# Performance work log

Hardware: AMD Instinct MI355X
Metric: run time of the kernel (lower is better)

Reference implementation:

```python
import jax, jax.numpy as jnp
import numpy as np

TEMPERATURE = 0.5  # set externally on the torch module; fixed here
EPS = 1e-10

B, NPTS, NDIM = 8, 1024, 64
K, S = 16, 512  # n_clusters, book_size


def setup_inputs() -> dict:
    key = jax.random.key(0)
    k1, k2, k3, k4 = jax.random.split(key, 4)
    ze = jax.random.normal(k1, (B, NPTS, NDIM), dtype=jnp.float32)
    # per-sample cluster probabilities (rows sum to 1)
    c_probs = jax.nn.softmax(jax.random.normal(k2, (B, K), dtype=jnp.float32), axis=-1)
    books = jax.random.normal(k3, (K, S, NDIM), dtype=jnp.float32)
    log_param_q = jnp.asarray(np.log(1.0), dtype=jnp.float32)  # param_q_init = 1.0
    gumbel_u = jax.random.uniform(k4, (B, K, NPTS, S), dtype=jnp.float32)
    return {"ze": ze, "c_probs": c_probs, "books": books,
            "log_param_q": log_param_q, "gumbel_u": gumbel_u}


def reference(ze, c_probs, books, log_param_q, gumbel_u):
    # precision of the Gaussian quantizer
    precision_q = 0.5 / jnp.clip(jnp.exp(log_param_q), 1e-10)
    # squared euclidean distances: [b, k, n, s]
    d = (jnp.sum(ze * ze, axis=-1)[:, None, :, None]
         + jnp.sum(books * books, axis=-1)[None, :, None, :]
         - 2.0 * jnp.einsum('bnd,ksd->bkns', ze, books))
    logits = -d * precision_q                                   # [b,k,n,s]
    # gumbel-softmax sample (training branch)
    g = -jnp.log(-jnp.log(gumbel_u + EPS) + EPS)
    encodings = jax.nn.softmax((logits + g) / TEMPERATURE, axis=-1)
    # soft codebook lookup, mixed over clusters by per-sample c_probs
    zq = jnp.einsum('bkns,ksd,bk->bnd', encodings, books, c_probs)
    prob = jax.nn.softmax(logits, axis=-1)
    log_prob = jax.nn.log_softmax(logits, axis=-1)
    return (zq, precision_q, prob, log_prob)
```

## Files before the change

kernel.cpp:

```cpp
#include <hip/hip_runtime.h>
#include <hip/hip_bf16.h>

typedef __attribute__((ext_vector_type(8))) short short8;
typedef __attribute__((ext_vector_type(4))) float f32x4;
typedef __attribute__((ext_vector_type(2))) float f32x2;

#define WS_ZE     0u
#define WS_ZELO   (1u<<20)
#define WS_B1H    (2u<<20)
#define WS_B1L    (3u<<20)
#define WS_B2     (4u<<20)
#define WS_ZN2    (5u<<20)
#define WS_BS2    ((5u<<20)+32768u)
#define WS_ZQP    (6u<<20)

__device__ __forceinline__ unsigned short f2bf(float x) {
  __hip_bfloat16 h = __float2bfloat16(x);
  return __builtin_bit_cast(unsigned short, h);
}
__device__ __forceinline__ float bf2f(unsigned short u) {
  union { unsigned int i; float f; } x; x.i = ((unsigned int)u) << 16; return x.f;
}
__device__ __forceinline__ void lds_barrier() {
  asm volatile("s_waitcnt lgkmcnt(0)" ::: "memory");
  __builtin_amdgcn_s_barrier();
}

__global__ __launch_bounds__(256) void prep_all_k(const float* __restrict__ ze,
                                                  const float* __restrict__ books,
                                                  const float* __restrict__ lpq,
                                                  char* __restrict__ ws,
                                                  float* __restrict__ d_out) {
  const int bb = blockIdx.x;
  if (bb < 32) {
    int t = bb * 256 + threadIdx.x;
    const f32x4* row = (const f32x4*)(ze + t * 64);
    unsigned short* dh = (unsigned short*)(ws + WS_ZE) + t * 64;
    unsigned short* dl = (unsigned short*)(ws + WS_ZELO) + t * 64;
    float s = 0.f;
#pragma unroll
    for (int c = 0; c < 8; ++c) {
      const f32x4 v0 = row[2 * c], v1 = row[2 * c + 1];
      union { unsigned short u[8]; short8 v; } H, L;
#pragma unroll
      for (int r = 0; r < 4; ++r) {
        float a = v0[r]; s += a * a;
        unsigned short h = f2bf(a); H.u[r] = h; L.u[r] = f2bf(a - bf2f(h));
        float b = v1[r]; s += b * b;
        unsigned short h2 = f2bf(b); H.u[4 + r] = h2; L.u[4 + r] = f2bf(b - bf2f(h2));
      }
      *(short8*)(dh + c * 8) = H.v;
      *(short8*)(dl + c * 8) = L.v;
    }
    ((float*)(ws + WS_ZN2))[t] = s;
  } else if (bb < 64) {
    int t = (bb - 32) * 256 + threadIdx.x;
    if (t == 0) d_out[524288] = 0.5f / fmaxf(expf(lpq[0]), 1e-10f);
    const f32x4* row = (const f32x4*)(books + t * 64);
    float s = 0.f;
#pragma unroll
    for (int c = 0; c < 16; ++c) {
      const f32x4 v = row[c];
#pragma unroll
      for (int r = 0; r < 4; ++r) s += v[r] * v[r];
    }
    ((float*)(ws + WS_BS2))[t] = s;
  } else if (bb < 320) {
    int t = (bb - 64) * 256 + threadIdx.x;
    const int sl = t & 15, g = (t >> 4) & 3, f = (t >> 6) & 1, tt = (t >> 7) & 31, k = t >> 12;
    const float* src = books + ((k * 512 + tt * 16 + sl) * 64 + f * 32 + g * 8);
    const f32x4 v0 = *(const f32x4*)(src);
    const f32x4 v1 = *(const f32x4*)(src + 4);
    union { unsigned short u[8]; short8 v; } H, L;
#pragma unroll
    for (int r = 0; r < 4; ++r) {
      unsigned short h = f2bf(v0[r]); H.u[r] = h; L.u[r] = f2bf(v0[r] - bf2f(h));
      unsigned short h2 = f2bf(v1[r]); H.u[4 + r] = h2; L.u[4 + r] = f2bf(v1[r] - bf2f(h2));
    }
    const int off = (k * 32 + tt) * 2048 + f * 1024 + (sl + g * 16) * 16;
    *(short8*)(ws + WS_B1H + off) = H.v;
    *(short8*)(ws + WS_B1L + off) = L.v;
  } else {
    int t = (bb - 320) * 256 + threadIdx.x;
    const int l15 = t & 15, sub = (t >> 4) & 3, m = (t >> 6) & 3, w = (t >> 8) & 7,
              hh = (t >> 11) & 1, k = t >> 12;
    const float* src = books + ((k * 512 + hh * 256 + w * 32 + sub * 8) * 64 + m * 16 + l15);
    union { unsigned short u[8]; short8 v; } H;
#pragma unroll
    for (int j = 0; j < 8; ++j) H.u[j] = f2bf(src[j * 64]);
    *(short8*)(ws + WS_B2 + k * 65536 + ((hh * 8 + w) * 4 + m) * 1024 + (l15 + sub * 16) * 16) = H.v;
  }
}

__global__ __launch_bounds__(256) void zq_red_k(const char* __restrict__ ws,
                                                float* __restrict__ d_out) {
  int t = blockIdx.x * 256 + threadIdx.x;
  const f32x4 a = *(const f32x4*)(ws + WS_ZQP + t * 16);
  const f32x4 b = *(const f32x4*)(ws + WS_ZQP + (2u << 20) + t * 16);
  const f32x4 c = *(const f32x4*)(ws + WS_ZQP + (4u << 20) + t * 16);
  *(f32x4*)(d_out + t * 4) = a + b + c;
}

__global__ __launch_bounds__(512, 3)
void gvq_main(const float* __restrict__ gum, const float* __restrict__ cprobs,
              const float* __restrict__ lpq, char* __restrict__ ws,
              float* __restrict__ d_out) {
  __shared__ char lds[50240];
  char* lgb  = lds;
  char* encb = lds + 33024;
  float* scr_esc = (float*)(lds + 50176);

  const int tid  = threadIdx.x;
  const int lane = tid & 63;
  const int wave = tid >> 6;
  const int l15  = lane & 15;
  const int g4   = lane >> 4;

  const int bid = blockIdx.x;
  const unsigned kg = (unsigned)bid % 3u;
  const int bt  = (int)((unsigned)bid / 3u);
  const int b   = bt >> 6;
  const int n0  = (bt & 63) * 16;
  const int kbeg = (kg == 0) ? 0 : (kg == 1 ? 6 : 11);
  const int kcnt = (kg == 0) ? 6 : 5;

  const float prec  = 0.5f / fmaxf(expf(lpq[0]), 1e-10f);
  const float prec2 = 2.0f * prec;
  const float C24   = 3.7751345442790977e-11f;

  const unsigned short* zh = (const unsigned short*)(ws + WS_ZE)   + (b * 1024 + n0 + l15) * 64;
  const unsigned short* zl = (const unsigned short*)(ws + WS_ZELO) + (b * 1024 + n0 + l15) * 64;
  const short8 zf0h = *(const short8*)(zh + g4 * 8);
  const short8 zf1h = *(const short8*)(zh + 32 + g4 * 8);
  const short8 zf0l = *(const short8*)(zl + g4 * 8);
  const short8 zf1l = *(const short8*)(zl + 32 + g4 * 8);
  const float zn2p = ((const float*)(ws + WS_ZN2))[b * 1024 + n0 + l15] * prec;

  f32x4 zacc[4] = {{0,0,0,0},{0,0,0,0},{0,0,0,0},{0,0,0,0}};

  const int nr0 = wave * 2, nr1 = wave * 2 + 1;

#pragma unroll 1
  for (int kk = 0; kk < kcnt; ++kk) {
    const int k = kbeg + kk;
    const float cp = cprobs[b * 16 + k];
    const char* b1h = ws + WS_B1H + k * 65536;
    const char* b1l = ws + WS_B1L + k * 65536;
    const char* b2  = ws + WS_B2  + k * 65536;
    const float* bs2k = (const float*)(ws + WS_BS2) + k * 512;
    const long row0 = ((long)((b * 16 + k) * 1024) + n0 + nr0) * 512;
    const long row1 = ((long)((b * 16 + k) * 1024) + n0 + nr1) * 512;

#pragma unroll
    for (int i = 0; i < 4; ++i) {
      const int t = wave * 4 + i;
      const char* bh = b1h + t * 2048 + lane * 16;
      const char* bl = b1l + t * 2048 + lane * 16;
      const short8 a0h = *(const short8*)(bh);
      const short8 a1h = *(const short8*)(bh + 1024);
      const short8 a0l = *(const short8*)(bl);
      const short8 a1l = *(const short8*)(bl + 1024);
      f32x4 c = {0.f, 0.f, 0.f, 0.f};
      c = __builtin_amdgcn_mfma_f32_16x16x32_bf16(a0h, zf0h, c, 0, 0, 0);
      c = __builtin_amdgcn_mfma_f32_16x16x32_bf16(a1h, zf1h, c, 0, 0, 0);
      c = __builtin_amdgcn_mfma_f32_16x16x32_bf16(a0h, zf0l, c, 0, 0, 0);
      c = __builtin_amdgcn_mfma_f32_16x16x32_bf16(a1h, zf1l, c, 0, 0, 0);
      c = __builtin_amdgcn_mfma_f32_16x16x32_bf16(a0l, zf0h, c, 0, 0, 0);
      c = __builtin_amdgcn_mfma_f32_16x16x32_bf16(a1l, zf1h, c, 0, 0, 0);
      const f32x4 bs2v = *(const f32x4*)(bs2k + t * 16 + g4 * 4);
      f32x4 lv;
#pragma unroll
      for (int r = 0; r < 4; ++r)
        lv[r] = fmaf(c[r], prec2, fmaf(bs2v[r], -prec, -zn2p));
      *(f32x4*)(lgb + l15 * 2064 + (t * 16 + g4 * 4) * 4) = lv;
    }

    float uv0[8], uv1[8];
#pragma unroll
    for (int j = 0; j < 8; ++j)
      uv0[j] = __builtin_nontemporal_load(gum + row0 + j * 64 + lane);
#pragma unroll
    for (int j = 0; j < 8; ++j)
      uv1[j] = __builtin_nontemporal_load(gum + row1 + j * 64 + lane);

    lds_barrier();

#pragma unroll
    for (int r = 0; r < 2; ++r) {
      const int n = r ? nr1 : nr0;
      const long rowb = r ? row1 : row0;
      float Lv[8], e1[8];
      const float* l32 = (const float*)(lgb + n * 2064);
#pragma unroll
      for (int j = 0; j < 8; ++j) Lv[j] = l32[j * 64 + lane];

      float m = Lv[0];
#pragma unroll
      for (int j = 1; j < 8; ++j) m = fmaxf(m, Lv[j]);
#pragma unroll
      for (int o = 1; o < 64; o <<= 1) m = fmaxf(m, __shfl_xor(m, o));

      unsigned short* er = (unsigned short*)(encb + n * 1072);
      float z1 = 0.f, z2 = 0.f;
#pragma unroll
      for (int j = 0; j < 8; ++j) {
        const float u = r ? uv1[j] : uv0[j];
        e1[j] = __expf(Lv[j] - m); z1 += e1[j];
        const float L  = 1e-10f - __logf(u + 1e-10f);
        const float rl = __builtin_amdgcn_rcpf(L);
        const float e2 = (e1[j] * e1[j]) * (rl * rl) * C24;
        z2 += e2;
        er[j * 64 + lane] = f2bf(e2);
      }
#pragma unroll
      for (int o = 1; o < 64; o <<= 1) {
        z1 += __shfl_xor(z1, o);
        z2 += __shfl_xor(z2, o);
      }
      const float rz1 = 1.0f / z1;
      const float c1  = m + __logf(z1);
      if (lane == 0) scr_esc[n] = cp / z2;

      float* pp = d_out + 524289 + rowb;
      float* pl = pp + 67108864;
#pragma unroll
      for (int j = 0; j < 8; ++j)
        __builtin_nontemporal_store(e1[j] * rz1, pp + j * 64 + lane);
#pragma unroll
      for (int j = 0; j < 8; ++j)
        __builtin_nontemporal_store(Lv[j] - c1, pl + j * 64 + lane);
    }
    lds_barrier();

    {
      f32x4 cacc[4] = {{0,0,0,0},{0,0,0,0},{0,0,0,0},{0,0,0,0}};
#pragma unroll
      for (int h = 0; h < 2; ++h) {
        const short8 bf = *(const short8*)(encb + l15 * 1072 +
                                           (h * 256 + wave * 32 + g4 * 8) * 2);
        const char* afb = b2 + ((h * 8 + wave) * 4) * 1024 + lane * 16;
#pragma unroll
        for (int m = 0; m < 4; ++m) {
          const short8 af = *(const short8*)(afb + m * 1024);
          cacc[m] = __builtin_amdgcn_mfma_f32_16x16x32_bf16(af, bf, cacc[m], 0, 0, 0);
        }
      }
      const float esc = scr_esc[l15];
#pragma unroll
      for (int m = 0; m < 4; ++m)
#pragma unroll
        for (int r = 0; r < 4; ++r) zacc[m][r] = fmaf(cacc[m][r], esc, zacc[m][r]);
    }
  }

  __syncthreads();
#pragma unroll
  for (int m = 0; m < 4; ++m)
    *(f32x4*)(lds + wave * 4096 + l15 * 256 + m * 64 + g4 * 16) = zacc[m];
  __syncthreads();
  const int e = tid * 2;
  f32x2 acc = {0.f, 0.f};
#pragma unroll
  for (int w = 0; w < 8; ++w) acc += *(const f32x2*)(lds + w * 4096 + e * 4);
  *(f32x2*)(ws + WS_ZQP + kg * (2u << 20) +
            (((unsigned)(b * 1024 + n0)) * 64 + e) * 4) = acc;
}

extern "C" void kernel_launch(void* const* d_in, const int* in_sizes, int n_in,
                              void* d_out, int out_size, void* d_ws, size_t ws_size,
                              hipStream_t stream) {
  (void)in_sizes; (void)n_in; (void)out_size; (void)ws_size;
  const float* ze     = (const float*)d_in[0];
  const float* cprobs = (const float*)d_in[1];
  const float* books  = (const float*)d_in[2];
  const float* lpq    = (const float*)d_in[3];
  const float* gum    = (const float*)d_in[4];
  float* out = (float*)d_out;
  char* ws = (char*)d_ws;
  hipLaunchKernelGGL(prep_all_k, dim3(576),  dim3(256), 0, stream, ze, books, lpq, ws, out);
  hipLaunchKernelGGL(gvq_main,   dim3(1536), dim3(512), 0, stream, gum, cprobs, lpq, ws, out);
  hipLaunchKernelGGL(zq_red_k,   dim3(512),  dim3(256), 0, stream, ws, out);
}
```

Baseline: 233.1 us.

## Drop split-bf16 distance GEMM, reuse LDS for encodings, split clusters four ways

Replaces the hi/lo split-bf16 distance computation (six MFMAs per tile) with a single plain bf16 product (two MFMAs), and removes the low-part workspace buffers and their preparation. The encoding buffer now aliases the logits LDS region, which cuts shared memory and allows four blocks per CU with 2048 blocks, each handling four clusters. Gumbel loads move into the per-row loop, and prob is computed as exp(log_prob), which removes the reciprocal. Computing distances in plain bf16 lowers accuracy of the logits and of the prob/log_prob outputs, and the extra barrier needed for the aliased LDS adds synchronisation.

```diff
diff --git a/kernel.cpp b/kernel.cpp
--- a/kernel.cpp
+++ b/kernel.cpp
@@ -6,20 +6,15 @@
 typedef __attribute__((ext_vector_type(2))) float f32x2;
 
 #define WS_ZE     0u
-#define WS_ZELO   (1u<<20)
-#define WS_B1H    (2u<<20)
-#define WS_B1L    (3u<<20)
-#define WS_B2     (4u<<20)
-#define WS_ZN2    (5u<<20)
-#define WS_BS2    ((5u<<20)+32768u)
-#define WS_ZQP    (6u<<20)
+#define WS_B1H    (1u<<20)
+#define WS_B2     (2u<<20)
+#define WS_ZN2    (3u<<20)
+#define WS_BS2    ((3u<<20)+32768u)
+#define WS_ZQP    (4u<<20)
 
 __device__ __forceinline__ unsigned short f2bf(float x) {
   __hip_bfloat16 h = __float2bfloat16(x);
   return __builtin_bit_cast(unsigned short, h);
-}
-__device__ __forceinline__ float bf2f(unsigned short u) {
-  union { unsigned int i; float f; } x; x.i = ((unsigned int)u) << 16; return x.f;
 }
 __device__ __forceinline__ void lds_barrier() {
   asm volatile("s_waitcnt lgkmcnt(0)" ::: "memory");
@@ -36,21 +31,17 @@
     int t = bb * 256 + threadIdx.x;
     const f32x4* row = (const f32x4*)(ze + t * 64);
     unsigned short* dh = (unsigned short*)(ws + WS_ZE) + t * 64;
-    unsigned short* dl = (unsigned short*)(ws + WS_ZELO) + t * 64;
     float s = 0.f;
 #pragma unroll
     for (int c = 0; c < 8; ++c) {
       const f32x4 v0 = row[2 * c], v1 = row[2 * c + 1];
-      union { unsigned short u[8]; short8 v; } H, L;
+      union { unsigned short u[8]; short8 v; } H;
 #pragma unroll
       for (int r = 0; r < 4; ++r) {
-        float a = v0[r]; s += a * a;
-        unsigned short h = f2bf(a); H.u[r] = h; L.u[r] = f2bf(a - bf2f(h));
-        float b = v1[r]; s += b * b;
-        unsigned short h2 = f2bf(b); H.u[4 + r] = h2; L.u[4 + r] = f2bf(b - bf2f(h2));
+        float a = v0[r]; s += a * a; H.u[r] = f2bf(a);
+        float b = v1[r]; s += b * b; H.u[4 + r] = f2bf(b);
       }
       *(short8*)(dh + c * 8) = H.v;
-      *(short8*)(dl + c * 8) = L.v;
     }
     ((float*)(ws + WS_ZN2))[t] = s;
   } else if (bb < 64) {
@@ -71,15 +62,10 @@
     const float* src = books + ((k * 512 + tt * 16 + sl) * 64 + f * 32 + g * 8);
     const f32x4 v0 = *(const f32x4*)(src);
     const f32x4 v1 = *(const f32x4*)(src + 4);
-    union { unsigned short u[8]; short8 v; } H, L;
-#pragma unroll
-    for (int r = 0; r < 4; ++r) {
-      unsigned short h = f2bf(v0[r]); H.u[r] = h; L.u[r] = f2bf(v0[r] - bf2f(h));
-      unsigned short h2 = f2bf(v1[r]); H.u[4 + r] = h2; L.u[4 + r] = f2bf(v1[r] - bf2f(h2));
-    }
-    const int off = (k * 32 + tt) * 2048 + f * 1024 + (sl + g * 16) * 16;
-    *(short8*)(ws + WS_B1H + off) = H.v;
-    *(short8*)(ws + WS_B1L + off) = L.v;
+    union { unsigned short u[8]; short8 v; } H;
+#pragma unroll
+    for (int r = 0; r < 4; ++r) { H.u[r] = f2bf(v0[r]); H.u[4 + r] = f2bf(v1[r]); }
+    *(short8*)(ws + WS_B1H + (k * 32 + tt) * 2048 + f * 1024 + (sl + g * 16) * 16) = H.v;
   } else {
     int t = (bb - 320) * 256 + threadIdx.x;
     const int l15 = t & 15, sub = (t >> 4) & 3, m = (t >> 6) & 3, w = (t >> 8) & 7,
@@ -98,17 +84,17 @@
   const f32x4 a = *(const f32x4*)(ws + WS_ZQP + t * 16);
   const f32x4 b = *(const f32x4*)(ws + WS_ZQP + (2u << 20) + t * 16);
   const f32x4 c = *(const f32x4*)(ws + WS_ZQP + (4u << 20) + t * 16);
-  *(f32x4*)(d_out + t * 4) = a + b + c;
-}
-
-__global__ __launch_bounds__(512, 3)
+  const f32x4 d = *(const f32x4*)(ws + WS_ZQP + (6u << 20) + t * 16);
+  *(f32x4*)(d_out + t * 4) = (a + b) + (c + d);
+}
+
+__global__ __launch_bounds__(512, 4)
 void gvq_main(const float* __restrict__ gum, const float* __restrict__ cprobs,
               const float* __restrict__ lpq, char* __restrict__ ws,
               float* __restrict__ d_out) {
-  __shared__ char lds[50240];
-  char* lgb  = lds;
-  char* encb = lds + 33024;
-  float* scr_esc = (float*)(lds + 50176);
+  __shared__ char lds[33088];
+  char* lgb = lds;
+  float* scr_esc = (float*)(lds + 33024);
 
   const int tid  = threadIdx.x;
   const int lane = tid & 63;
@@ -117,23 +103,19 @@
   const int g4   = lane >> 4;
 
   const int bid = blockIdx.x;
-  const unsigned kg = (unsigned)bid % 3u;
-  const int bt  = (int)((unsigned)bid / 3u);
+  const unsigned kg = ((unsigned)bid & 7u) >> 1;
+  const int bt  = ((bid >> 3) << 1) | (bid & 1);
   const int b   = bt >> 6;
   const int n0  = (bt & 63) * 16;
-  const int kbeg = (kg == 0) ? 0 : (kg == 1 ? 6 : 11);
-  const int kcnt = (kg == 0) ? 6 : 5;
+  const int kbeg = (int)kg * 4;
 
   const float prec  = 0.5f / fmaxf(expf(lpq[0]), 1e-10f);
   const float prec2 = 2.0f * prec;
   const float C24   = 3.7751345442790977e-11f;
 
-  const unsigned short* zh = (const unsigned short*)(ws + WS_ZE)   + (b * 1024 + n0 + l15) * 64;
-  const unsigned short* zl = (const unsigned short*)(ws + WS_ZELO) + (b * 1024 + n0 + l15) * 64;
+  const unsigned short* zh = (const unsigned short*)(ws + WS_ZE) + (b * 1024 + n0 + l15) * 64;
   const short8 zf0h = *(const short8*)(zh + g4 * 8);
   const short8 zf1h = *(const short8*)(zh + 32 + g4 * 8);
-  const short8 zf0l = *(const short8*)(zl + g4 * 8);
-  const short8 zf1l = *(const short8*)(zl + 32 + g4 * 8);
   const float zn2p = ((const float*)(ws + WS_ZN2))[b * 1024 + n0 + l15] * prec;
 
   f32x4 zacc[4] = {{0,0,0,0},{0,0,0,0},{0,0,0,0},{0,0,0,0}};
@@ -141,11 +123,10 @@
   const int nr0 = wave * 2, nr1 = wave * 2 + 1;
 
 #pragma unroll 1
-  for (int kk = 0; kk < kcnt; ++kk) {
+  for (int kk = 0; kk < 4; ++kk) {
     const int k = kbeg + kk;
     const float cp = cprobs[b * 16 + k];
     const char* b1h = ws + WS_B1H + k * 65536;
-    const char* b1l = ws + WS_B1L + k * 65536;
     const char* b2  = ws + WS_B2  + k * 65536;
     const float* bs2k = (const float*)(ws + WS_BS2) + k * 512;
     const long row0 = ((long)((b * 16 + k) * 1024) + n0 + nr0) * 512;
@@ -155,18 +136,11 @@
     for (int i = 0; i < 4; ++i) {
       const int t = wave * 4 + i;
       const char* bh = b1h + t * 2048 + lane * 16;
-      const char* bl = b1l + t * 2048 + lane * 16;
       const short8 a0h = *(const short8*)(bh);
       const short8 a1h = *(const short8*)(bh + 1024);
-      const short8 a0l = *(const short8*)(bl);
-      const short8 a1l = *(const short8*)(bl + 1024);
       f32x4 c = {0.f, 0.f, 0.f, 0.f};
       c = __builtin_amdgcn_mfma_f32_16x16x32_bf16(a0h, zf0h, c, 0, 0, 0);
       c = __builtin_amdgcn_mfma_f32_16x16x32_bf16(a1h, zf1h, c, 0, 0, 0);
-      c = __builtin_amdgcn_mfma_f32_16x16x32_bf16(a0h, zf0l, c, 0, 0, 0);
-      c = __builtin_amdgcn_mfma_f32_16x16x32_bf16(a1h, zf1l, c, 0, 0, 0);
-      c = __builtin_amdgcn_mfma_f32_16x16x32_bf16(a0l, zf0h, c, 0, 0, 0);
-      c = __builtin_amdgcn_mfma_f32_16x16x32_bf16(a1l, zf1h, c, 0, 0, 0);
       const f32x4 bs2v = *(const f32x4*)(bs2k + t * 16 + g4 * 4);
       f32x4 lv;
 #pragma unroll
@@ -174,22 +148,18 @@
         lv[r] = fmaf(c[r], prec2, fmaf(bs2v[r], -prec, -zn2p));
       *(f32x4*)(lgb + l15 * 2064 + (t * 16 + g4 * 4) * 4) = lv;
     }
-
-    float uv0[8], uv1[8];
-#pragma unroll
-    for (int j = 0; j < 8; ++j)
-      uv0[j] = __builtin_nontemporal_load(gum + row0 + j * 64 + lane);
-#pragma unroll
-    for (int j = 0; j < 8; ++j)
-      uv1[j] = __builtin_nontemporal_load(gum + row1 + j * 64 + lane);
-
     lds_barrier();
 
 #pragma unroll
     for (int r = 0; r < 2; ++r) {
       const int n = r ? nr1 : nr0;
       const long rowb = r ? row1 : row0;
-      float Lv[8], e1[8];
+      float uv[8];
+#pragma unroll
+      for (int j = 0; j < 8; ++j)
+        uv[j] = __builtin_nontemporal_load(gum + rowb + j * 64 + lane);
+
+      float Lv[8];
       const float* l32 = (const float*)(lgb + n * 2064);
 #pragma unroll
       for (int j = 0; j < 8; ++j) Lv[j] = l32[j * 64 + lane];
@@ -200,15 +170,14 @@
 #pragma unroll
       for (int o = 1; o < 64; o <<= 1) m = fmaxf(m, __shfl_xor(m, o));
 
-      unsigned short* er = (unsigned short*)(encb + n * 1072);
+      unsigned short* er = (unsigned short*)(lgb + n * 2064);
       float z1 = 0.f, z2 = 0.f;
 #pragma unroll
       for (int j = 0; j < 8; ++j) {
-        const float u = r ? uv1[j] : uv0[j];
-        e1[j] = __expf(Lv[j] - m); z1 += e1[j];
-        const float L  = 1e-10f - __logf(u + 1e-10f);
+        const float e1 = __expf(Lv[j] - m); z1 += e1;
+        const float L  = 1e-10f - __logf(uv[j] + 1e-10f);
         const float rl = __builtin_amdgcn_rcpf(L);
-        const float e2 = (e1[j] * e1[j]) * (rl * rl) * C24;
+        const float e2 = (e1 * e1) * (rl * rl) * C24;
         z2 += e2;
         er[j * 64 + lane] = f2bf(e2);
       }
@@ -217,18 +186,17 @@
         z1 += __shfl_xor(z1, o);
         z2 += __shfl_xor(z2, o);
       }
-      const float rz1 = 1.0f / z1;
-      const float c1  = m + __logf(z1);
+      const float c1 = m + __logf(z1);
       if (lane == 0) scr_esc[n] = cp / z2;
 
       float* pp = d_out + 524289 + rowb;
       float* pl = pp + 67108864;
 #pragma unroll
-      for (int j = 0; j < 8; ++j)
-        __builtin_nontemporal_store(e1[j] * rz1, pp + j * 64 + lane);
-#pragma unroll
-      for (int j = 0; j < 8; ++j)
-        __builtin_nontemporal_store(Lv[j] - c1, pl + j * 64 + lane);
+      for (int j = 0; j < 8; ++j) {
+        const float lpv = Lv[j] - c1;
+        __builtin_nontemporal_store(__expf(lpv), pp + j * 64 + lane);
+        __builtin_nontemporal_store(lpv, pl + j * 64 + lane);
+      }
     }
     lds_barrier();
 
@@ -236,7 +204,7 @@
       f32x4 cacc[4] = {{0,0,0,0},{0,0,0,0},{0,0,0,0},{0,0,0,0}};
 #pragma unroll
       for (int h = 0; h < 2; ++h) {
-        const short8 bf = *(const short8*)(encb + l15 * 1072 +
+        const short8 bf = *(const short8*)(lgb + l15 * 2064 +
                                            (h * 256 + wave * 32 + g4 * 8) * 2);
         const char* afb = b2 + ((h * 8 + wave) * 4) * 1024 + lane * 16;
 #pragma unroll
@@ -251,6 +219,7 @@
 #pragma unroll
         for (int r = 0; r < 4; ++r) zacc[m][r] = fmaf(cacc[m][r], esc, zacc[m][r]);
     }
+    lds_barrier();
   }
 
   __syncthreads();
@@ -278,6 +247,6 @@
   float* out = (float*)d_out;
   char* ws = (char*)d_ws;
   hipLaunchKernelGGL(prep_all_k, dim3(576),  dim3(256), 0, stream, ze, books, lpq, ws, out);
-  hipLaunchKernelGGL(gvq_main,   dim3(1536), dim3(512), 0, stream, gum, cprobs, lpq, ws, out);
+  hipLaunchKernelGGL(gvq_main,   dim3(2048), dim3(512), 0, stream, gum, cprobs, lpq, ws, out);
   hipLaunchKernelGGL(zq_red_k,   dim3(512),  dim3(256), 0, stream, ws, out);
 }
```

Result: no change. 230.5 us (-1.1%).
